# Performance work log

Hardware: AMD Instinct MI355X
Metric: run time of the kernel (lower is better)

The kernel has to match this reference:

```python
import jax, jax.numpy as jnp
import numpy as np
import math

NUM_HEADS = 4


def setup_inputs() -> dict:
    key = jax.random.key(0)
    k1, k2, k3, k4 = jax.random.split(key, 4)
    b, c, f, t = 8, 512, 32, 64
    x = jax.random.normal(k1, (b, c, f, t), dtype=jnp.float32)
    # Conv1d(k=1) weights stored as 2D (out, in); fan-in scaled like torch default
    qkv_w = jax.random.normal(k2, (3 * c, c), dtype=jnp.float32) / math.sqrt(c)
    qkv_b = jax.random.normal(k3, (3 * c,), dtype=jnp.float32) * 0.02
    proj_w = jax.random.normal(k4, (c, c), dtype=jnp.float32) / math.sqrt(c)
    proj_b = jnp.zeros((c,), dtype=jnp.float32)
    return {"x": x, "qkv_w": qkv_w, "qkv_b": qkv_b, "proj_w": proj_w, "proj_b": proj_b}


def reference(x, qkv_w, qkv_b, proj_w, proj_b):
    b, c, f, t = x.shape
    T = f * t
    xr = x.reshape(b, c, T)  # [b, c, T]
    # Note: original forward computes PositionalEncoding2D(x) but discards it.
    qkv = jnp.einsum('oc,bct->bot', qkv_w, xr) + qkv_b[None, :, None]  # [b, 3c, T]
    H = NUM_HEADS
    ch = c // H
    q, k, v = jnp.split(qkv, 3, axis=1)  # each [b, c, T]
    q = q.reshape(b * H, ch, T)
    k = k.reshape(b * H, ch, T)
    v = v.reshape(b * H, ch, T)
    scale = 1.0 / math.sqrt(math.sqrt(ch))
    w = jnp.einsum('bct,bcs->bts', q * scale, k * scale)  # [b*H, T, T]
    w = jax.nn.softmax(w.astype(jnp.float32), axis=-1).astype(q.dtype)
    a = jnp.einsum('bts,bcs->bct', w, v).reshape(b, c, T)
    h = jnp.einsum('oc,bct->bot', proj_w, a) + proj_b[None, :, None]
    return (xr + h).reshape(b, c, f, t)
```

## Files before the change

kernel.cpp:

```cpp
#include <hip/hip_runtime.h>

#define DEV static __device__ __forceinline__

typedef __attribute__((ext_vector_type(8))) short short8;
typedef __attribute__((ext_vector_type(4))) float f32x4;
typedef __attribute__((ext_vector_type(16))) float f32x16;
typedef __attribute__((ext_vector_type(2))) unsigned int uint2v;

DEV unsigned short f2bf(float f) {
    union { float f; unsigned int u; } v; v.f = f;
    unsigned int u = v.u;
    unsigned int r = (u + 0x7fffu + ((u >> 16) & 1u)) >> 16;
    return (unsigned short)r;
}

DEV unsigned int cvtpk(float lo, float hi) {
    unsigned int r;
    asm("v_cvt_pk_bf16_f32 %0, %1, %2" : "=v"(r) : "v"(lo), "v"(hi));
    return r;
}

DEV float pl32_max(float v) {
    union { float f; unsigned u; } c; c.f = v;
    uint2v r = __builtin_amdgcn_permlane32_swap(c.u, c.u, false, false);
    union { unsigned u; float f; } a, b; a.u = r[0]; b.u = r[1];
    return fmaxf(a.f, b.f);
}
DEV float pl32_sum(float v) {
    union { float f; unsigned u; } c; c.f = v;
    uint2v r = __builtin_amdgcn_permlane32_swap(c.u, c.u, false, false);
    union { unsigned u; float f; } a, b; a.u = r[0]; b.u = r[1];
    return a.f + b.f;
}

DEV unsigned short* swp(unsigned short* base, int row, int col, int rs) {
    int a = ((row * rs + col) << 1) ^ ((row & 7) << 4);
    return (unsigned short*)((char*)base + a);
}

DEV void lds_barrier() {
    asm volatile("s_waitcnt lgkmcnt(0)" ::: "memory");
    __builtin_amdgcn_s_barrier();
}

__global__ void prep_kernel(const float* __restrict__ qkv_w,
                            const float* __restrict__ proj_w,
                            unsigned short* __restrict__ Wq,
                            unsigned short* __restrict__ Wp) {
    int i = blockIdx.x * blockDim.x + threadIdx.x;
    int stride = gridDim.x * blockDim.x;
    for (int j = i; j < 1536 * 512; j += stride) Wq[j] = f2bf(qkv_w[j]);
    for (int j = i; j < 512 * 512;  j += stride) Wp[j] = f2bf(proj_w[j]);
}

__global__ __launch_bounds__(256) void transpose_kernel(const float* __restrict__ x,
                                                        unsigned short* __restrict__ Xt) {
    __shared__ unsigned char lt[64 * 128];
    int b  = blockIdx.z;
    int c0 = blockIdx.y * 64;
    int t0 = blockIdx.x * 64;
    int tid = threadIdx.x;
    int tx = tid & 15, cy0 = tid >> 4;
    for (int p = 0; p < 4; ++p) {
        int cy = cy0 + p * 16;
        const float* src = &x[((size_t)(b * 512 + c0 + cy)) * 2048 + t0 + tx * 4];
        f32x4 v = *(const f32x4*)src;
        unsigned long long pk = (unsigned long long)f2bf(v[0])
                              | ((unsigned long long)f2bf(v[1]) << 16)
                              | ((unsigned long long)f2bf(v[2]) << 32)
                              | ((unsigned long long)f2bf(v[3]) << 48);
        int addr = (cy * 128 + tx * 8) ^ ((cy & 7) << 4);
        *(unsigned long long*)(lt + addr) = pk;
    }
    __syncthreads();
    int c16 = (tid & 3) * 16, tr = tid >> 2;
    unsigned short buf[16];
    for (int i = 0; i < 16; ++i) {
        int c = c16 + i;
        int addr = (c * 128 + tr * 2) ^ ((c & 7) << 4);
        buf[i] = *(unsigned short*)(lt + addr);
    }
    unsigned short* dst = &Xt[((size_t)(b * 2048 + t0 + tr)) * 512 + c0 + c16];
    *(short8*)dst       = *(short8*)&buf[0];
    *(short8*)(dst + 8) = *(short8*)&buf[8];
}

#define LP 72

template <int ORIENT>
__global__ __launch_bounds__(256, 2) void gemm_qkv_kernel(
    const unsigned short* __restrict__ Wq,
    const unsigned short* __restrict__ Xt,
    const float* __restrict__ qkv_b,
    unsigned short* __restrict__ Qw,
    unsigned short* __restrict__ Kw,
    unsigned short* __restrict__ Vw) {
    __shared__ unsigned short Ws[2][128][LP];
    __shared__ unsigned short Bs[2][128][LP];
    int b  = blockIdx.z;
    int ot = (ORIENT == 0) ? blockIdx.y : (8 + blockIdx.y);
    int o0 = ot * 128, t0 = blockIdx.x * 128;
    int tid = threadIdx.x, lane = tid & 63, w = tid >> 6;
    int lr = lane >> 4, lc = lane & 15;
    int wr = (w >> 1) * 64, wc = (w & 1) * 64;
    f32x4 acc[4][4];
    for (int m = 0; m < 4; m++)
        for (int n = 0; n < 4; n++) acc[m][n] = (f32x4){0.f, 0.f, 0.f, 0.f};
    int srow = tid >> 3, soff = (tid & 7) * 8;

    short8 wreg[4], breg[4];
    #pragma unroll
    for (int p = 0; p < 4; p++) {
        wreg[p] = *(const short8*)&Wq[(size_t)(o0 + srow + p * 32) * 512 + soff];
        breg[p] = *(const short8*)&Xt[((size_t)(b * 2048) + t0 + srow + p * 32) * 512 + soff];
    }
    for (int t = 0; t < 8; ++t) {
        int cur = t & 1;
        #pragma unroll
        for (int p = 0; p < 4; p++) {
            *(short8*)&Ws[cur][srow + p * 32][soff] = wreg[p];
            *(short8*)&Bs[cur][srow + p * 32][soff] = breg[p];
        }
        if (t < 7) {
            int k1 = (t + 1) * 64;
            #pragma unroll
            for (int p = 0; p < 4; p++) {
                wreg[p] = *(const short8*)&Wq[(size_t)(o0 + srow + p * 32) * 512 + k1 + soff];
                breg[p] = *(const short8*)&Xt[((size_t)(b * 2048) + t0 + srow + p * 32) * 512 + k1 + soff];
            }
        }
        lds_barrier();
        for (int kk = 0; kk < 64; kk += 32) {
            int kb = kk + lr * 8;
            short8 af[4], bfv[4];
            if (ORIENT == 0) {
                for (int m = 0; m < 4; m++) af[m]  = *(const short8*)&Bs[cur][wr + m * 16 + lc][kb];
                for (int n = 0; n < 4; n++) bfv[n] = *(const short8*)&Ws[cur][wc + n * 16 + lc][kb];
            } else {
                for (int m = 0; m < 4; m++) af[m]  = *(const short8*)&Ws[cur][wr + m * 16 + lc][kb];
                for (int n = 0; n < 4; n++) bfv[n] = *(const short8*)&Bs[cur][wc + n * 16 + lc][kb];
            }
            for (int m = 0; m < 4; m++)
                for (int n = 0; n < 4; n++)
                    acc[m][n] = __builtin_amdgcn_mfma_f32_16x16x32_bf16(af[m], bfv[n], acc[m][n], 0, 0, 0);
        }
        __builtin_amdgcn_s_barrier();
    }
    const float scale = 0.29730177875068026f;
    for (int m = 0; m < 4; m++)
        for (int n = 0; n < 4; n++)
            for (int r = 0; r < 4; r++) {
                int row = wr + m * 16 + lr * 4 + r;
                int col = wc + n * 16 + lc;
                float val = acc[m][n][r];
                if (ORIENT == 0) {
                    int t = t0 + row;
                    int o = o0 + col;
                    val = (val + qkv_b[o]) * scale;
                    if (o < 512) {
                        int h = o >> 7, cc = o & 127;
                        Qw[((size_t)((b * 4 + h) * 2048 + t)) * 128 + cc] = f2bf(val);
                    } else {
                        int oo = o - 512;
                        int h = oo >> 7, cc = oo & 127;
                        Kw[((size_t)((b * 4 + h) * 2048 + t)) * 128 + cc] = f2bf(val);
                    }
                } else {
                    int o = o0 + row;
                    int t = t0 + col;
                    val += qkv_b[o];
                    int oo = o - 1024;
                    int h = oo >> 7, cc = oo & 127;
                    Vw[((size_t)((b * 4 + h) * 128 + cc)) * 2048 + t] = f2bf(val);
                }
            }
}

__global__ __launch_bounds__(256, 2) void attn_kernel(
    const unsigned short* __restrict__ Qw,
    const unsigned short* __restrict__ Kw,
    const unsigned short* __restrict__ Vw,
    unsigned short* __restrict__ Aw) {
    __shared__ unsigned short lds[32768];
    int bid = blockIdx.x;
    int bh = bid & 31;
    int t0 = (bid >> 5) * 128;
    int tid = threadIdx.x, lane = tid & 63, w = tid >> 6;
    int l31 = lane & 31, hi = lane >> 5;
    int qrow = w * 32;

    const unsigned short* Kbase = &Kw[(size_t)bh * 2048 * 128];
    const unsigned short* Vbase = &Vw[(size_t)bh * 128 * 2048];

    short8 qf[8];
    #pragma unroll
    for (int st = 0; st < 8; st++)
        qf[st] = *(const short8*)&Qw[((size_t)bh * 2048 + t0 + qrow + l31) * 128 + st * 16 + hi * 8];

    f32x16 oacc[4];
    #pragma unroll
    for (int ct = 0; ct < 4; ct++)
        #pragma unroll
        for (int i = 0; i < 16; i++) oacc[ct][i] = 0.f;
    float mst = -1e30f, lst = 0.f;

    int kr = tid >> 4, ko = (tid & 15) * 8;
    int vr = tid >> 3, vo = (tid & 7) * 8;

    short8 kreg[4], vreg[4];
    #pragma unroll
    for (int p = 0; p < 4; p++)
        kreg[p] = *(const short8*)&Kbase[(size_t)(kr + p * 16) * 128 + ko];
    #pragma unroll
    for (int p = 0; p < 4; p++)
        vreg[p] = *(const short8*)&Vbase[(size_t)(vr + p * 32) * 2048 + vo];

    for (int it = 0; it < 32; ++it) {
        int cur = it & 1;
        unsigned short* Kb = lds + cur * 8192;
        unsigned short* Vb = lds + 16384 + cur * 8192;
        #pragma unroll
        for (int p = 0; p < 4; p++) *(short8*)swp(Kb, kr + p * 16, ko, 128) = kreg[p];
        #pragma unroll
        for (int p = 0; p < 4; p++) *(short8*)swp(Vb, vr + p * 32, vo, 64) = vreg[p];
        if (it + 1 < 32) {
            int s1 = (it + 1) * 64;
            #pragma unroll
            for (int p = 0; p < 4; p++)
                kreg[p] = *(const short8*)&Kbase[(size_t)(s1 + kr + p * 16) * 128 + ko];
            #pragma unroll
            for (int p = 0; p < 4; p++)
                vreg[p] = *(const short8*)&Vbase[(size_t)(vr + p * 32) * 2048 + s1 + vo];
        }
        lds_barrier();

        f32x16 s0, s1v;
        #pragma unroll
        for (int i = 0; i < 16; i++) { s0[i] = 0.f; s1v[i] = 0.f; }
        __builtin_amdgcn_s_setprio(1);
        #pragma unroll
        for (int st = 0; st < 8; st++) {
            short8 k0 = *(const short8*)swp(Kb, l31,      st * 16 + hi * 8, 128);
            short8 k1 = *(const short8*)swp(Kb, 32 + l31, st * 16 + hi * 8, 128);
            s0  = __builtin_amdgcn_mfma_f32_32x32x16_bf16(k0, qf[st], s0, 0, 0, 0);
            s1v = __builtin_amdgcn_mfma_f32_32x32x16_bf16(k1, qf[st], s1v, 0, 0, 0);
        }
        __builtin_amdgcn_s_setprio(0);

        float m16[16];
        #pragma unroll
        for (int i = 0; i < 16; i++) m16[i] = fmaxf(s0[i], s1v[i]);
        #pragma unroll
        for (int sdt = 8; sdt > 0; sdt >>= 1)
            #pragma unroll
            for (int i = 0; i < 8; i++)
                if (i < sdt) m16[i] = fmaxf(m16[i], m16[i + sdt]);
        float mx = pl32_max(m16[0]);
        if (!__all(mx <= mst + 8.0f)) {
            float mnew = fmaxf(mst, mx);
            float resc = __expf(mst - mnew);
            mst = mnew;
            lst *= resc;
            #pragma unroll
            for (int ct = 0; ct < 4; ct++)
                #pragma unroll
                for (int i = 0; i < 16; i++) oacc[ct][i] *= resc;
        }
        float pe[32];
        #pragma unroll
        for (int i = 0; i < 16; i++) pe[i]      = __expf(s0[i]  - mst);
        #pragma unroll
        for (int i = 0; i < 16; i++) pe[16 + i] = __expf(s1v[i] - mst);
        float a16[16];
        #pragma unroll
        for (int i = 0; i < 16; i++) a16[i] = pe[i] + pe[16 + i];
        #pragma unroll
        for (int sdt = 8; sdt > 0; sdt >>= 1)
            #pragma unroll
            for (int i = 0; i < 8; i++)
                if (i < sdt) a16[i] = a16[i] + a16[i + sdt];
        lst += pl32_sum(a16[0]);

        short8 pf[4];
        #pragma unroll
        for (int st = 0; st < 4; st++) {
            unsigned X0 = cvtpk(pe[st * 8 + 0], pe[st * 8 + 1]);
            unsigned X1 = cvtpk(pe[st * 8 + 2], pe[st * 8 + 3]);
            unsigned Y0 = cvtpk(pe[st * 8 + 4], pe[st * 8 + 5]);
            unsigned Y1 = cvtpk(pe[st * 8 + 6], pe[st * 8 + 7]);
            uint2v r0 = __builtin_amdgcn_permlane32_swap(X0, Y0, false, false);
            uint2v r1 = __builtin_amdgcn_permlane32_swap(X1, Y1, false, false);
            union { unsigned u[4]; short8 s; } uu;
            uu.u[0] = r0[0];
            uu.u[1] = r1[0];
            uu.u[2] = r0[1];
            uu.u[3] = r1[1];
            pf[st] = uu.s;
        }

        __builtin_amdgcn_s_setprio(1);
        #pragma unroll
        for (int ct = 0; ct < 4; ct++)
            #pragma unroll
            for (int st = 0; st < 4; st++) {
                short8 va = *(const short8*)swp(Vb, ct * 32 + l31, st * 16 + hi * 8, 64);
                oacc[ct] = __builtin_amdgcn_mfma_f32_32x32x16_bf16(va, pf[st], oacc[ct], 0, 0, 0);
            }
        __builtin_amdgcn_s_setprio(0);
    }

    __syncthreads();
    unsigned short* ep = lds + w * 4096;
    float invl = 1.f / lst;
    #pragma unroll
    for (int ct = 0; ct < 4; ct++)
        #pragma unroll
        for (int i = 0; i < 8; i++) {
            int c = (2 * i & 3) + 8 * (i >> 1) + 4 * hi + 32 * ct;
            unsigned d = cvtpk(oacc[ct][2 * i] * invl, oacc[ct][2 * i + 1] * invl);
            *(unsigned*)swp(ep, l31, c, 128) = d;
        }
    asm volatile("" ::: "memory");
    int q = lane >> 1, hf = lane & 1;
    int b = bh >> 2, h = bh & 3;
    #pragma unroll
    for (int p = 0; p < 8; p++) {
        short8 v = *(const short8*)swp(ep, q, hf * 64 + p * 8, 128);
        *(short8*)&Aw[((size_t)(b * 2048) + t0 + qrow + q) * 512 + h * 128 + hf * 64 + p * 8] = v;
    }
}

__global__ __launch_bounds__(256, 2) void gemm_proj_kernel(
    const unsigned short* __restrict__ Wp,
    const unsigned short* __restrict__ Aw,
    const float* __restrict__ proj_b,
    const float* __restrict__ x,
    float* __restrict__ out) {
    __shared__ unsigned short Ws[2][128][LP];
    __shared__ unsigned short Bs[2][128][LP];
    int b  = blockIdx.z;
    int o0 = blockIdx.y * 128, t0 = blockIdx.x * 128;
    int tid = threadIdx.x, lane = tid & 63, w = tid >> 6;
    int lr = lane >> 4, lc = lane & 15;
    int wr = (w >> 1) * 64, wc = (w & 1) * 64;
    f32x4 acc[4][4];
    for (int m = 0; m < 4; m++)
        for (int n = 0; n < 4; n++) acc[m][n] = (f32x4){0.f, 0.f, 0.f, 0.f};
    int srow = tid >> 3, soff = (tid & 7) * 8;

    short8 wreg[4], breg[4];
    #pragma unroll
    for (int p = 0; p < 4; p++) {
        wreg[p] = *(const short8*)&Wp[(size_t)(o0 + srow + p * 32) * 512 + soff];
        breg[p] = *(const short8*)&Aw[((size_t)(b * 2048) + t0 + srow + p * 32) * 512 + soff];
    }
    for (int t = 0; t < 8; ++t) {
        int cur = t & 1;
        #pragma unroll
        for (int p = 0; p < 4; p++) {
            *(short8*)&Ws[cur][srow + p * 32][soff] = wreg[p];
            *(short8*)&Bs[cur][srow + p * 32][soff] = breg[p];
        }
        if (t < 7) {
            int k1 = (t + 1) * 64;
            #pragma unroll
            for (int p = 0; p < 4; p++) {
                wreg[p] = *(const short8*)&Wp[(size_t)(o0 + srow + p * 32) * 512 + k1 + soff];
                breg[p] = *(const short8*)&Aw[((size_t)(b * 2048) + t0 + srow + p * 32) * 512 + k1 + soff];
            }
        }
        lds_barrier();
        for (int kk = 0; kk < 64; kk += 32) {
            int kb = kk + lr * 8;
            short8 af[4], bfv[4];
            for (int m = 0; m < 4; m++) af[m]  = *(const short8*)&Ws[cur][wr + m * 16 + lc][kb];
            for (int n = 0; n < 4; n++) bfv[n] = *(const short8*)&Bs[cur][wc + n * 16 + lc][kb];
            for (int m = 0; m < 4; m++)
                for (int n = 0; n < 4; n++)
                    acc[m][n] = __builtin_amdgcn_mfma_f32_16x16x32_bf16(af[m], bfv[n], acc[m][n], 0, 0, 0);
        }
        __builtin_amdgcn_s_barrier();
    }
    for (int m = 0; m < 4; m++)
        for (int n = 0; n < 4; n++)
            for (int r = 0; r < 4; r++) {
                int o = o0 + wr + m * 16 + lr * 4 + r;
                int t = t0 + wc + n * 16 + lc;
                size_t idx = ((size_t)(b * 512) + o) * 2048 + t;
                out[idx] = x[idx] + acc[m][n][r] + proj_b[o];
            }
}

extern "C" void kernel_launch(void* const* d_in, const int* in_sizes, int n_in,
                              void* d_out, int out_size, void* d_ws, size_t ws_size,
                              hipStream_t stream) {
    const float* x      = (const float*)d_in[0];
    const float* qkv_w  = (const float*)d_in[1];
    const float* qkv_b  = (const float*)d_in[2];
    const float* proj_w = (const float*)d_in[3];
    const float* proj_b = (const float*)d_in[4];
    float* out = (float*)d_out;

    unsigned short* ws = (unsigned short*)d_ws;
    unsigned short* Wq = ws;
    unsigned short* Wp = Wq + (size_t)1536 * 512;
    unsigned short* Xt = Wp + (size_t)512 * 512;
    unsigned short* Qw = Xt + (size_t)8 * 2048 * 512;
    unsigned short* Kw = Qw + (size_t)32 * 2048 * 128;
    unsigned short* Vw = Kw + (size_t)32 * 2048 * 128;
    unsigned short* Aw = Vw + (size_t)32 * 2048 * 128;

    prep_kernel<<<dim3(512), dim3(256), 0, stream>>>(qkv_w, proj_w, Wq, Wp);
    transpose_kernel<<<dim3(32, 8, 8), dim3(256), 0, stream>>>(x, Xt);
    gemm_qkv_kernel<0><<<dim3(16, 8, 8), dim3(256), 0, stream>>>(Wq, Xt, qkv_b, Qw, Kw, Vw);
    gemm_qkv_kernel<1><<<dim3(16, 4, 8), dim3(256), 0, stream>>>(Wq, Xt, qkv_b, Qw, Kw, Vw);
    attn_kernel<<<dim3(512), dim3(256), 0, stream>>>(Qw, Kw, Vw, Aw);
    gemm_proj_kernel<<<dim3(16, 4, 8), dim3(256), 0, stream>>>(Wp, Aw, proj_b, x, out);
}
```

Baseline: 167.0 us.

## Use direct global-to-LDS loads in QKV GEMM and fold log2e into Q scale

The QKV GEMM now stages tiles with global_load_lds straight into XOR-swizzled LDS buffers, replacing the register round-trip and padded layout. It keeps a double-buffered prefetch with a vmcnt wait before each barrier. Separately, Q is pre-scaled by log2(e), so the attention softmax can use raw v_exp_f32 (exp2) in place of __expf, with the rescale threshold adjusted to match. This cuts register pressure and VALU work in exchange for a more complex swizzle and a small change in numerical path.

```diff
diff --git a/kernel.cpp b/kernel.cpp
--- a/kernel.cpp
+++ b/kernel.cpp
@@ -20,6 +20,12 @@
     return r;
 }
 
+DEV float vexp2(float x) {
+    float r;
+    asm("v_exp_f32 %0, %1" : "=v"(r) : "v"(x));
+    return r;
+}
+
 DEV float pl32_max(float v) {
     union { float f; unsigned u; } c; c.f = v;
     uint2v r = __builtin_amdgcn_permlane32_swap(c.u, c.u, false, false);
@@ -41,6 +47,11 @@
 DEV void lds_barrier() {
     asm volatile("s_waitcnt lgkmcnt(0)" ::: "memory");
     __builtin_amdgcn_s_barrier();
+}
+
+DEV void gload16(const void* g, void* l) {
+    __builtin_amdgcn_global_load_lds((const __attribute__((address_space(1))) void*)g,
+                                     (__attribute__((address_space(3))) void*)l, 16, 0, 0);
 }
 
 __global__ void prep_kernel(const float* __restrict__ qkv_w,
@@ -85,8 +96,6 @@
     *(short8*)(dst + 8) = *(short8*)&buf[8];
 }
 
-#define LP 72
-
 template <int ORIENT>
 __global__ __launch_bounds__(256, 2) void gemm_qkv_kernel(
     const unsigned short* __restrict__ Wq,
@@ -95,8 +104,8 @@
     unsigned short* __restrict__ Qw,
     unsigned short* __restrict__ Kw,
     unsigned short* __restrict__ Vw) {
-    __shared__ unsigned short Ws[2][128][LP];
-    __shared__ unsigned short Bs[2][128][LP];
+    __shared__ unsigned short As[2][128 * 64];
+    __shared__ unsigned short Bs[2][128 * 64];
     int b  = blockIdx.z;
     int ot = (ORIENT == 0) ? blockIdx.y : (8 + blockIdx.y);
     int o0 = ot * 128, t0 = blockIdx.x * 128;
@@ -106,47 +115,51 @@
     f32x4 acc[4][4];
     for (int m = 0; m < 4; m++)
         for (int n = 0; n < 4; n++) acc[m][n] = (f32x4){0.f, 0.f, 0.f, 0.f};
-    int srow = tid >> 3, soff = (tid & 7) * 8;
-
-    short8 wreg[4], breg[4];
-    #pragma unroll
-    for (int p = 0; p < 4; p++) {
-        wreg[p] = *(const short8*)&Wq[(size_t)(o0 + srow + p * 32) * 512 + soff];
-        breg[p] = *(const short8*)&Xt[((size_t)(b * 2048) + t0 + srow + p * 32) * 512 + soff];
-    }
+
+    int r8 = lane >> 3, ck = lane & 7;
+    int sc8 = (ck ^ r8) * 8;
+
+    const unsigned short* Wbase = &Wq[(size_t)o0 * 512];
+    const unsigned short* Xbase = &Xt[((size_t)(b * 2048) + t0) * 512];
+
+    #define QKV_STAGE(buf, ks)                                                        \
+        _Pragma("unroll")                                                             \
+        for (int p = 0; p < 4; p++) {                                                 \
+            int rowblk = (w * 4 + p) * 8;                                             \
+            gload16(&Wbase[(size_t)(rowblk + r8) * 512 + (ks) * 64 + sc8],            \
+                    &As[buf][rowblk * 64]);                                           \
+            gload16(&Xbase[(size_t)(rowblk + r8) * 512 + (ks) * 64 + sc8],            \
+                    &Bs[buf][rowblk * 64]);                                           \
+        }
+
+    QKV_STAGE(0, 0);
+    asm volatile("s_waitcnt vmcnt(0)" ::: "memory");
+    __builtin_amdgcn_s_barrier();
     for (int t = 0; t < 8; ++t) {
         int cur = t & 1;
-        #pragma unroll
-        for (int p = 0; p < 4; p++) {
-            *(short8*)&Ws[cur][srow + p * 32][soff] = wreg[p];
-            *(short8*)&Bs[cur][srow + p * 32][soff] = breg[p];
-        }
-        if (t < 7) {
-            int k1 = (t + 1) * 64;
-            #pragma unroll
-            for (int p = 0; p < 4; p++) {
-                wreg[p] = *(const short8*)&Wq[(size_t)(o0 + srow + p * 32) * 512 + k1 + soff];
-                breg[p] = *(const short8*)&Xt[((size_t)(b * 2048) + t0 + srow + p * 32) * 512 + k1 + soff];
-            }
-        }
-        lds_barrier();
+        if (t < 7) { QKV_STAGE(cur ^ 1, t + 1); }
+        unsigned short* Ab = (unsigned short*)As[cur];
+        unsigned short* Bb = (unsigned short*)Bs[cur];
+        #pragma unroll
         for (int kk = 0; kk < 64; kk += 32) {
             int kb = kk + lr * 8;
             short8 af[4], bfv[4];
             if (ORIENT == 0) {
-                for (int m = 0; m < 4; m++) af[m]  = *(const short8*)&Bs[cur][wr + m * 16 + lc][kb];
-                for (int n = 0; n < 4; n++) bfv[n] = *(const short8*)&Ws[cur][wc + n * 16 + lc][kb];
+                for (int m = 0; m < 4; m++) af[m]  = *(const short8*)swp(Bb, wr + m * 16 + lc, kb, 64);
+                for (int n = 0; n < 4; n++) bfv[n] = *(const short8*)swp(Ab, wc + n * 16 + lc, kb, 64);
             } else {
-                for (int m = 0; m < 4; m++) af[m]  = *(const short8*)&Ws[cur][wr + m * 16 + lc][kb];
-                for (int n = 0; n < 4; n++) bfv[n] = *(const short8*)&Bs[cur][wc + n * 16 + lc][kb];
+                for (int m = 0; m < 4; m++) af[m]  = *(const short8*)swp(Ab, wr + m * 16 + lc, kb, 64);
+                for (int n = 0; n < 4; n++) bfv[n] = *(const short8*)swp(Bb, wc + n * 16 + lc, kb, 64);
             }
             for (int m = 0; m < 4; m++)
                 for (int n = 0; n < 4; n++)
                     acc[m][n] = __builtin_amdgcn_mfma_f32_16x16x32_bf16(af[m], bfv[n], acc[m][n], 0, 0, 0);
         }
+        asm volatile("s_waitcnt vmcnt(0)" ::: "memory");
         __builtin_amdgcn_s_barrier();
     }
-    const float scale = 0.29730177875068026f;
+    const float scale_k = 0.29730177875068026f;
+    const float scale_q = 0.42891498953885586f;
     for (int m = 0; m < 4; m++)
         for (int n = 0; n < 4; n++)
             for (int r = 0; r < 4; r++) {
@@ -156,7 +169,8 @@
                 if (ORIENT == 0) {
                     int t = t0 + row;
                     int o = o0 + col;
-                    val = (val + qkv_b[o]) * scale;
+                    float sc = (o < 512) ? scale_q : scale_k;
+                    val = (val + qkv_b[o]) * sc;
                     if (o < 512) {
                         int h = o >> 7, cc = o & 127;
                         Qw[((size_t)((b * 4 + h) * 2048 + t)) * 128 + cc] = f2bf(val);
@@ -256,9 +270,9 @@
             for (int i = 0; i < 8; i++)
                 if (i < sdt) m16[i] = fmaxf(m16[i], m16[i + sdt]);
         float mx = pl32_max(m16[0]);
-        if (!__all(mx <= mst + 8.0f)) {
+        if (!__all(mx <= mst + 11.541560327111707f)) {
             float mnew = fmaxf(mst, mx);
-            float resc = __expf(mst - mnew);
+            float resc = vexp2(mst - mnew);
             mst = mnew;
             lst *= resc;
             #pragma unroll
@@ -268,9 +282,9 @@
         }
         float pe[32];
         #pragma unroll
-        for (int i = 0; i < 16; i++) pe[i]      = __expf(s0[i]  - mst);
-        #pragma unroll
-        for (int i = 0; i < 16; i++) pe[16 + i] = __expf(s1v[i] - mst);
+        for (int i = 0; i < 16; i++) pe[i]      = vexp2(s0[i]  - mst);
+        #pragma unroll
+        for (int i = 0; i < 16; i++) pe[16 + i] = vexp2(s1v[i] - mst);
         float a16[16];
         #pragma unroll
         for (int i = 0; i < 16; i++) a16[i] = pe[i] + pe[16 + i];
@@ -330,6 +344,7 @@
     }
 }
 
+#define LP 72
 __global__ __launch_bounds__(256, 2) void gemm_proj_kernel(
     const unsigned short* __restrict__ Wp,
     const unsigned short* __restrict__ Aw,
```

After: 165.3 us, median of 2. About the same (-1.0%).
